# Optimization experiments

Measured on AMD Instinct MI355X. Metric: run time of the kernel, lower is better.

The kernel has to match this reference:

```python
import jax, jax.numpy as jnp
import numpy as np

RADIUS, HEAD, SLOT, DIM = 16.0, 8, 112, 512

def _l2norm(x, axis):
    n = jnp.linalg.norm(x, axis=axis, keepdims=True)
    return x / jnp.maximum(n, 1e-12)

def _layernorm(x, g, b, eps=1e-5):
    mu = jnp.mean(x, axis=-1, keepdims=True)
    var = jnp.mean((x - mu) ** 2, axis=-1, keepdims=True)
    return (x - mu) / jnp.sqrt(var + eps) * g + b

def setup_inputs() -> dict:
    key = jax.random.key(0)
    ks = jax.random.split(key, 12)
    B, S = 32, 512
    return {
        "query": jax.random.normal(ks[0], (B, S, DIM), jnp.float32),
        "value": jax.random.normal(ks[1], (B, S, DIM), jnp.float32),
        "key_mem": jax.random.normal(ks[2], (HEAD * SLOT, DIM // HEAD), jnp.float32) * 0.5,
        "value_mem": jax.random.normal(ks[3], (SLOT, DIM), jnp.float32) * 0.5,
        "Wq": jax.random.normal(ks[4], (DIM, DIM), jnp.float32) * 0.02,
        "bq": jnp.zeros((DIM,), jnp.float32),
        "Wv": jax.random.normal(ks[5], (DIM, DIM), jnp.float32) * 0.02,
        "bv": jnp.zeros((DIM,), jnp.float32),
        "Wl": jax.random.normal(ks[6], (DIM, DIM * HEAD), jnp.float32) * 0.02,
        "bl": jnp.zeros((DIM,), jnp.float32),
        "g1": jnp.ones((DIM,), jnp.float32), "b1": jnp.zeros((DIM,), jnp.float32),
        "g2": jnp.ones((DIM,), jnp.float32), "b2": jnp.zeros((DIM,), jnp.float32),
        "g3": jnp.ones((DIM,), jnp.float32), "b3": jnp.zeros((DIM,), jnp.float32),
    }

def reference(query, value, key_mem, value_mem, Wq, bq, Wv, bv, Wl, bl,
              g1, b1, g2, b2, g3, b3):
    B, S, C = query.shape
    mq = query.reshape(B * S, C)                                   # (BS, 512)
    # --- key addressing (read path) ---
    key_norm = _l2norm(key_mem.reshape(HEAD, SLOT, -1), axis=2)    # (h, s, 64)
    eq = _l2norm((mq @ Wq.T + bq).reshape(B * S, HEAD, -1), axis=2)
    key_sim = jnp.einsum('bhd,hsd->bhs', eq, key_norm)             # (BS, h, s)
    key_add = jax.nn.softmax(RADIUS * key_sim, axis=2)
    m_head = jnp.einsum('bhs,sd->bhd', key_add,
                        jax.lax.stop_gradient(value_mem))          # (BS, h, 512)
    vir = _layernorm(m_head.reshape(B * S, HEAD * DIM) @ Wl.T + bl, g2, b2)
    te_fusion = _layernorm(query + vir.reshape(B, S, DIM), g1, b1)  # dropout = eval identity
    # --- value addressing (write/train path) ---
    mv = value.reshape(B * S, DIM)
    ev = jax.lax.stop_gradient(mv) @ Wv.T + bv
    value_norm = _l2norm(value_mem, axis=1)                        # (s, 512)
    value_sim = _l2norm(ev, axis=1) @ value_norm.T                 # (BS, s)
    value_add = jax.nn.softmax(RADIUS * value_sim, axis=1)
    aud = value_add @ value_mem                                    # (BS, 512)
    contrastive = 0.5 * jnp.abs(jnp.eye(SLOT, dtype=value_norm.dtype)
                                - value_norm @ value_norm.T).sum()[None]
    mvd = jax.lax.stop_gradient(mv)
    cos = (aud * mvd).sum(1) / jnp.maximum(
        jnp.linalg.norm(aud, axis=1) * jnp.linalg.norm(mvd, axis=1), 1e-8)
    recon = jnp.abs(1.0 - cos).reshape(B, S).sum(1)                # (B,)
    aud = _layernorm(aud, g3, b3)
    tr_fusion = _layernorm(query + aud.reshape(B, S, DIM), g1, b1)
    return (te_fusion, tr_fusion, recon, contrastive)
```

## Files before the change

### kernel.cpp

```cpp
#include <hip/hip_runtime.h>
#include <math.h>

#define DIMC   512
#define HEADS  8
#define SLOTS  112
#define HD     64
#define NROWS  16384
#define RADIUSF 16.0f

typedef short short8 __attribute__((ext_vector_type(8)));
typedef unsigned short ushort8 __attribute__((ext_vector_type(8)));
typedef float f32x4  __attribute__((ext_vector_type(4)));

__device__ __forceinline__ unsigned short f2bf(float f)
{
    unsigned u = __float_as_uint(f);
    unsigned r = (u + 0x7FFFu + ((u >> 16) & 1u)) >> 16;
    return (unsigned short)r;
}
__device__ __forceinline__ float bf2f(unsigned short h)
{
    return __uint_as_float((unsigned)h << 16);
}

__device__ __forceinline__ void gl16(const void* g, void* lds_wave_base)
{
    __builtin_amdgcn_global_load_lds(
        (const __attribute__((address_space(1))) unsigned int*)g,
        (__attribute__((address_space(3))) unsigned int*)lds_wave_base,
        16, 0, 0);
}

#define DPP_ADD(x, ctrl, rmask)                                               \
    (x) += __int_as_float(__builtin_amdgcn_update_dpp(                        \
               0, __float_as_int(x), (ctrl), (rmask), 0xf, true))

__device__ __forceinline__ float wsum64(float x)
{
    DPP_ADD(x, 0x111, 0xf);
    DPP_ADD(x, 0x112, 0xf);
    DPP_ADD(x, 0x114, 0xf);
    DPP_ADD(x, 0x118, 0xf);
    DPP_ADD(x, 0x142, 0xa);
    DPP_ADD(x, 0x143, 0xc);
    return __int_as_float(__builtin_amdgcn_readlane(__float_as_int(x), 63));
}

__device__ __forceinline__ void wsum64_4(float& a, float& b, float& c, float& d)
{
    DPP_ADD(a, 0x111, 0xf); DPP_ADD(b, 0x111, 0xf); DPP_ADD(c, 0x111, 0xf); DPP_ADD(d, 0x111, 0xf);
    DPP_ADD(a, 0x112, 0xf); DPP_ADD(b, 0x112, 0xf); DPP_ADD(c, 0x112, 0xf); DPP_ADD(d, 0x112, 0xf);
    DPP_ADD(a, 0x114, 0xf); DPP_ADD(b, 0x114, 0xf); DPP_ADD(c, 0x114, 0xf); DPP_ADD(d, 0x114, 0xf);
    DPP_ADD(a, 0x118, 0xf); DPP_ADD(b, 0x118, 0xf); DPP_ADD(c, 0x118, 0xf); DPP_ADD(d, 0x118, 0xf);
    DPP_ADD(a, 0x142, 0xa); DPP_ADD(b, 0x142, 0xa); DPP_ADD(c, 0x142, 0xa); DPP_ADD(d, 0x142, 0xa);
    DPP_ADD(a, 0x143, 0xc); DPP_ADD(b, 0x143, 0xc); DPP_ADD(c, 0x143, 0xc); DPP_ADD(d, 0x143, 0xc);
    a = __int_as_float(__builtin_amdgcn_readlane(__float_as_int(a), 63));
    b = __int_as_float(__builtin_amdgcn_readlane(__float_as_int(b), 63));
    c = __int_as_float(__builtin_amdgcn_readlane(__float_as_int(c), 63));
    d = __int_as_float(__builtin_amdgcn_readlane(__float_as_int(d), 63));
}

__global__ __launch_bounds__(256)
void gemm_bf16(const short* __restrict__ A, int lda,
               const short* __restrict__ B, int ldb,
               float* __restrict__ C, unsigned short* __restrict__ Cb,
               int ldc, int K, const float* __restrict__ bias, int Nvalid,
               int aZ, int bZ, int cZ)
{
    __shared__ short As[128 * 32];
    __shared__ short Bs[128 * 32];
    A += (size_t)blockIdx.z * aZ;
    B += (size_t)blockIdx.z * bZ;
    const size_t czoff = (size_t)blockIdx.z * cZ;
    const int tid  = threadIdx.x;
    const int wave = tid >> 6;
    const int lane = tid & 63;
    const int m0 = blockIdx.y * 128;
    const int n0 = blockIdx.x * 128;
    const int wm = (wave >> 1) * 64;
    const int wn = (wave & 1) * 64;

    const int srow = tid >> 2;
    const int schk = (tid & 3) * 8;

    const int fr = lane & 15;
    const int fq = (lane >> 4) * 8;

    f32x4 acc[4][4] = {};

    const short* Ag = A + (size_t)(m0 + srow) * lda + schk;
    const short* Bg = B + (size_t)(n0 + srow) * ldb + schk;

    short* asL = As + wave * 512;
    short* asU = As + 2048 + wave * 512;
    short* bsL = Bs + wave * 512;
    short* bsU = Bs + 2048 + wave * 512;

    for (int k0 = 0; k0 < K; k0 += 32) {
        gl16(Ag, asL);
        gl16(Ag + (size_t)64 * lda, asU);
        gl16(Bg, bsL);
        gl16(Bg + (size_t)64 * ldb, bsU);
        Ag += 32; Bg += 32;
        __syncthreads();
        short8 af[4], bf[4];
        #pragma unroll
        for (int i = 0; i < 4; ++i)
            af[i] = *(const short8*)&As[(wm + i * 16 + fr) * 32 + fq];
        #pragma unroll
        for (int j = 0; j < 4; ++j)
            bf[j] = *(const short8*)&Bs[(wn + j * 16 + fr) * 32 + fq];
        #pragma unroll
        for (int i = 0; i < 4; ++i)
            #pragma unroll
            for (int j = 0; j < 4; ++j)
                acc[i][j] = __builtin_amdgcn_mfma_f32_16x16x32_bf16(
                    af[i], bf[j], acc[i][j], 0, 0, 0);
        __syncthreads();
    }

    const int cr = (lane >> 4) * 4;
    const int cc = lane & 15;
    #pragma unroll
    for (int i = 0; i < 4; ++i) {
        const int grow = m0 + wm + i * 16 + cr;
        #pragma unroll
        for (int j = 0; j < 4; ++j) {
            const int gcol = n0 + wn + j * 16 + cc;
            if (gcol < Nvalid) {
                const float bb = bias ? bias[gcol] : 0.f;
                const size_t base = czoff + (size_t)grow * ldc + gcol;
                #pragma unroll
                for (int r = 0; r < 4; ++r) {
                    const float val = acc[i][j][r] + bb;
                    if (C)  C[base + (size_t)r * ldc]  = val;
                    if (Cb) Cb[base + (size_t)r * ldc] = f2bf(val);
                }
            }
        }
    }
}

__global__ __launch_bounds__(256)
void gemm_softmax(const short* __restrict__ A, int lda, int aZ,
                  const short* __restrict__ B, int ldb, int bZ,
                  int K,
                  unsigned short* __restrict__ Ob, int ldo, int oPerZ, int padN)
{
    __shared__ short As[128 * 32];
    __shared__ short Bs[128 * 32];
    __shared__ float P[128][113];
    __shared__ float hinvS[128];
    A += (size_t)blockIdx.z * aZ;
    B += (size_t)blockIdx.z * bZ;
    const int tid  = threadIdx.x;
    const int wave = tid >> 6;
    const int lane = tid & 63;
    const int m0 = blockIdx.y * 128;
    const int wm = (wave >> 1) * 64;
    const int wn = (wave & 1) * 64;
    const int srow = tid >> 2;
    const int schk = (tid & 3) * 8;
    const int fr = lane & 15;
    const int fq = (lane >> 4) * 8;

    f32x4 acc[4][4] = {};
    float ss[4] = {0.f, 0.f, 0.f, 0.f};

    const short* Ag = A + (size_t)(m0 + srow) * lda + schk;
    const short* Bg = B + (size_t)srow * ldb + schk;

    short* asL = As + wave * 512;
    short* asU = As + 2048 + wave * 512;
    short* bsL = Bs + wave * 512;
    short* bsU = Bs + 2048 + wave * 512;

    for (int k0 = 0; k0 < K; k0 += 32) {
        gl16(Ag, asL);
        gl16(Ag + (size_t)64 * lda, asU);
        gl16(Bg, bsL);
        gl16(Bg + (size_t)64 * ldb, bsU);
        Ag += 32; Bg += 32;
        __syncthreads();
        short8 af[4], bf[4];
        #pragma unroll
        for (int i = 0; i < 4; ++i)
            af[i] = *(const short8*)&As[(wm + i * 16 + fr) * 32 + fq];
        #pragma unroll
        for (int j = 0; j < 4; ++j)
            bf[j] = *(const short8*)&Bs[(wn + j * 16 + fr) * 32 + fq];
        #pragma unroll
        for (int i = 0; i < 4; ++i)
            #pragma unroll
            for (int e = 0; e < 8; ++e) {
                const float f = bf2f((unsigned short)af[i][e]);
                ss[i] += f * f;
            }
        #pragma unroll
        for (int i = 0; i < 4; ++i)
            #pragma unroll
            for (int j = 0; j < 4; ++j)
                acc[i][j] = __builtin_amdgcn_mfma_f32_16x16x32_bf16(
                    af[i], bf[j], acc[i][j], 0, 0, 0);
        __syncthreads();
    }

    #pragma unroll
    for (int i = 0; i < 4; ++i) {
        ss[i] += __shfl_xor(ss[i], 16, 64);
        ss[i] += __shfl_xor(ss[i], 32, 64);
    }
    if (lane < 16) {
        #pragma unroll
        for (int i = 0; i < 4; ++i)
            hinvS[wm + i * 16 + lane] = 1.f / fmaxf(sqrtf(ss[i]), 1e-12f);
    }

    const int cr = (lane >> 4) * 4;
    const int cc = lane & 15;
    #pragma unroll
    for (int i = 0; i < 4; ++i) {
        const int prow = wm + i * 16 + cr;
        #pragma unroll
        for (int j = 0; j < 4; ++j) {
            const int pcol = wn + j * 16 + cc;
            if (pcol < SLOTS) {
                #pragma unroll
                for (int r = 0; r < 4; ++r)
                    P[prow + r][pcol] = acc[i][j][r];
            }
        }
    }
    __syncthreads();

    const int rowt = tid >> 1;
    const int half = tid & 1;
    const int k0 = half * 56;
    const int rr = m0 + rowt;
    const float s = RADIUSF * hinvS[rowt];
    float mx = -1e30f;
    for (int k = k0; k < k0 + 56; ++k) mx = fmaxf(mx, P[rowt][k]);
    mx = fmaxf(mx, __shfl_xor(mx, 1, 64));
    float sum = 0.f;
    for (int k = k0; k < k0 + 56; ++k) {
        const float e = __expf(s * (P[rowt][k] - mx));
        P[rowt][k] = e;
        sum += e;
    }
    sum += __shfl_xor(sum, 1, 64);
    const float inv = 1.f / sum;
    unsigned short* orow = Ob + (size_t)rr * ldo + (size_t)blockIdx.z * oPerZ;
    for (int k = k0; k < k0 + 56; ++k) orow[k] = f2bf(P[rowt][k] * inv);
    if (half == 1)
        for (int k = SLOTS; k < padN; ++k) orow[k] = 0;
}


#define FUSED_GEMM_CORE(A, lda, B, ldb, K)                                    \
    f32x4 acc[2][8] = {};                                                     \
    {                                                                         \
        const int lrow = lane >> 2;                                           \
        const int lchk = (lane & 3) * 8;                                      \
        const short* Ag = (A) + (size_t)(m0 + wave * 16 + lrow) * (lda) + lchk;\
        const short* Bg = (B) + (size_t)(wave * 16 + lrow) * (ldb) + lchk;    \
        short* asB = As + wave * 512;                                         \
        short* bsB = Bs + wave * 512;                                         \
        for (int k0 = 0; k0 < (K); k0 += 32) {                                \
            if (wave < 2) gl16(Ag, asB);                                      \
            _Pragma("unroll")                                                 \
            for (int s = 0; s < 8; ++s)                                       \
                gl16(Bg + (size_t)(s * 64) * (ldb), bsB + s * 2048);          \
            Ag += 32; Bg += 32;                                               \
            __syncthreads();                                                  \
            short8 af[2], bf[8];                                              \
            af[0] = *(const short8*)&As[fr * 32 + fq];                        \
            af[1] = *(const short8*)&As[(16 + fr) * 32 + fq];                 \
            _Pragma("unroll")                                                 \
            for (int c = 0; c < 8; ++c)                                       \
                bf[c] = *(const short8*)&Bs[(wave * 128 + c * 16 + fr) * 32 + fq];\
            _Pragma("unroll")                                                 \
            for (int i = 0; i < 2; ++i)                                       \
                _Pragma("unroll")                                             \
                for (int c = 0; c < 8; ++c)                                   \
                    acc[i][c] = __builtin_amdgcn_mfma_f32_16x16x32_bf16(      \
                        af[i], bf[c], acc[i][c], 0, 0, 0);                    \
            __syncthreads();                                                  \
        }                                                                     \
    }                                                                         \
    {                                                                         \
        const int cr = (lane >> 4) * 4;                                       \
        const int cc = lane & 15;                                             \
        _Pragma("unroll")                                                     \
        for (int i = 0; i < 2; ++i)                                           \
            _Pragma("unroll")                                                 \
            for (int c = 0; c < 8; ++c) {                                     \
                const int col = wave * 128 + c * 16 + cc;                     \
                _Pragma("unroll")                                             \
                for (int r = 0; r < 4; ++r)                                   \
                    P[(i * 16 + cr + r) * 516 + col] = acc[i][c][r];          \
            }                                                                 \
    }                                                                         \
    __syncthreads();

__global__ __launch_bounds__(256)
void gemm_vir_te(const short* __restrict__ A, int lda,
                 const short* __restrict__ B, int ldb, int K,
                 const float* __restrict__ bias, const float* __restrict__ query,
                 const float* __restrict__ g1, const float* __restrict__ b1,
                 const float* __restrict__ g2, const float* __restrict__ b2,
                 float* __restrict__ out_te)
{
    __shared__ float P[32 * 516];
    short* As = (short*)P;
    short* Bs = As + 1024;
    const int tid = threadIdx.x;
    const int wave = tid >> 6;
    const int lane = tid & 63;
    const int m0 = blockIdx.x * 32;
    const int fr = lane & 15;
    const int fq = (lane >> 4) * 8;

    FUSED_GEMM_CORE(A, lda, B, ldb, K)

    const int c0 = lane * 8;
    float blv[8], gg2[8], bb2[8], gg1[8], bb1[8];
    *(f32x4*)&blv[0] = *(const f32x4*)(bias + c0);
    *(f32x4*)&blv[4] = *(const f32x4*)(bias + c0 + 4);
    *(f32x4*)&gg2[0] = *(const f32x4*)(g2 + c0);
    *(f32x4*)&gg2[4] = *(const f32x4*)(g2 + c0 + 4);
    *(f32x4*)&bb2[0] = *(const f32x4*)(b2 + c0);
    *(f32x4*)&bb2[4] = *(const f32x4*)(b2 + c0 + 4);
    *(f32x4*)&gg1[0] = *(const f32x4*)(g1 + c0);
    *(f32x4*)&gg1[4] = *(const f32x4*)(g1 + c0 + 4);
    *(f32x4*)&bb1[0] = *(const f32x4*)(b1 + c0);
    *(f32x4*)&bb1[4] = *(const f32x4*)(b1 + c0 + 4);

    for (int rp = 0; rp < 4; ++rp) {
        const int lr0 = rp * 8 + wave * 2;
        float x[2][8], q[2][8];
        #pragma unroll
        for (int p = 0; p < 2; ++p) {
            *(f32x4*)&x[p][0] = *(const f32x4*)&P[(lr0 + p) * 516 + c0];
            *(f32x4*)&x[p][4] = *(const f32x4*)&P[(lr0 + p) * 516 + c0 + 4];
            const size_t gbase = (size_t)(m0 + lr0 + p) * DIMC + c0;
            *(f32x4*)&q[p][0] = *(const f32x4*)(query + gbase);
            *(f32x4*)&q[p][4] = *(const f32x4*)(query + gbase + 4);
            #pragma unroll
            for (int j = 0; j < 8; ++j) x[p][j] += blv[j];
        }
        float s1[2] = {0.f, 0.f}, s2[2] = {0.f, 0.f};
        #pragma unroll
        for (int p = 0; p < 2; ++p)
            #pragma unroll
            for (int j = 0; j < 8; ++j) {
                s1[p] += x[p][j];
                s2[p] += x[p][j] * x[p][j];
            }
        wsum64_4(s1[0], s2[0], s1[1], s2[1]);

        float y[2][8];
        float t1[2] = {0.f, 0.f}, t2[2] = {0.f, 0.f};
        #pragma unroll
        for (int p = 0; p < 2; ++p) {
            const float mu = s1[p] * (1.f / DIMC);
            const float var = s2[p] * (1.f / DIMC) - mu * mu;
            const float rstd = rsqrtf(var + 1e-5f);
            #pragma unroll
            for (int j = 0; j < 8; ++j) {
                const float v = (x[p][j] - mu) * rstd * gg2[j] + bb2[j];
                y[p][j] = q[p][j] + v;
                t1[p] += y[p][j];
                t2[p] += y[p][j] * y[p][j];
            }
        }
        wsum64_4(t1[0], t2[0], t1[1], t2[1]);

        #pragma unroll
        for (int p = 0; p < 2; ++p) {
            const float mu = t1[p] * (1.f / DIMC);
            const float var = t2[p] * (1.f / DIMC) - mu * mu;
            const float rstd = rsqrtf(var + 1e-5f);
            float o[8];
            #pragma unroll
            for (int j = 0; j < 8; ++j)
                o[j] = (y[p][j] - mu) * rstd * gg1[j] + bb1[j];
            const size_t gbase = (size_t)(m0 + lr0 + p) * DIMC + c0;
            *(float4*)(out_te + gbase)     = make_float4(o[0], o[1], o[2], o[3]);
            *(float4*)(out_te + gbase + 4) = make_float4(o[4], o[5], o[6], o[7]);
        }
    }
}

__global__ __launch_bounds__(256)
void gemm_aud_tr(const short* __restrict__ A, int lda,
                 const short* __restrict__ B, int ldb, int K,
                 const float* __restrict__ value, const float* __restrict__ query,
                 const float* __restrict__ g1, const float* __restrict__ b1,
                 const float* __restrict__ g3, const float* __restrict__ b3,
                 float* __restrict__ out_tr, float* __restrict__ recon)
{
    __shared__ float P[32 * 516];
    __shared__ float red[4];
    short* As = (short*)P;
    short* Bs = As + 1024;
    const int tid = threadIdx.x;
    const int wave = tid >> 6;
    const int lane = tid & 63;
    const int m0 = blockIdx.x * 32;
    const int fr = lane & 15;
    const int fq = (lane >> 4) * 8;

    FUSED_GEMM_CORE(A, lda, B, ldb, K)

    const int c0 = lane * 8;
    float gg3[8], bb3[8], gg1[8], bb1[8];
    *(f32x4*)&gg3[0] = *(const f32x4*)(g3 + c0);
    *(f32x4*)&gg3[4] = *(const f32x4*)(g3 + c0 + 4);
    *(f32x4*)&bb3[0] = *(const f32x4*)(b3 + c0);
    *(f32x4*)&bb3[4] = *(const f32x4*)(b3 + c0 + 4);
    *(f32x4*)&gg1[0] = *(const f32x4*)(g1 + c0);
    *(f32x4*)&gg1[4] = *(const f32x4*)(g1 + c0 + 4);
    *(f32x4*)&bb1[0] = *(const f32x4*)(b1 + c0);
    *(f32x4*)&bb1[4] = *(const f32x4*)(b1 + c0 + 4);

    float rloc = 0.f;
    for (int rp = 0; rp < 4; ++rp) {
        const int lr0 = rp * 8 + wave * 2;
        float a[2][8], v[2][8], q[2][8];
        #pragma unroll
        for (int p = 0; p < 2; ++p) {
            *(f32x4*)&a[p][0] = *(const f32x4*)&P[(lr0 + p) * 516 + c0];
            *(f32x4*)&a[p][4] = *(const f32x4*)&P[(lr0 + p) * 516 + c0 + 4];
            const size_t gbase = (size_t)(m0 + lr0 + p) * DIMC + c0;
            *(f32x4*)&v[p][0] = *(const f32x4*)(value + gbase);
            *(f32x4*)&v[p][4] = *(const f32x4*)(value + gbase + 4);
            *(f32x4*)&q[p][0] = *(const f32x4*)(query + gbase);
            *(f32x4*)&q[p][4] = *(const f32x4*)(query + gbase + 4);
        }
        float dot[2] = {0.f, 0.f}, na[2] = {0.f, 0.f};
        float nv[2] = {0.f, 0.f}, s1[2] = {0.f, 0.f};
        #pragma unroll
        for (int p = 0; p < 2; ++p)
            #pragma unroll
            for (int j = 0; j < 8; ++j) {
                dot[p] += a[p][j] * v[p][j];
                na[p]  += a[p][j] * a[p][j];
                nv[p]  += v[p][j] * v[p][j];
                s1[p]  += a[p][j];
            }
        wsum64_4(dot[0], na[0], nv[0], s1[0]);
        wsum64_4(dot[1], na[1], nv[1], s1[1]);

        #pragma unroll
        for (int p = 0; p < 2; ++p) {
            const float cosv = dot[p] / fmaxf(sqrtf(na[p]) * sqrtf(nv[p]), 1e-8f);
            rloc += fabsf(1.f - cosv);
        }

        float y[2][8];
        float t1[2] = {0.f, 0.f}, t2[2] = {0.f, 0.f};
        #pragma unroll
        for (int p = 0; p < 2; ++p) {
            const float mu = s1[p] * (1.f / DIMC);
            const float var = na[p] * (1.f / DIMC) - mu * mu;
            const float rstd = rsqrtf(var + 1e-5f);
            #pragma unroll
            for (int j = 0; j < 8; ++j) {
                const float w = (a[p][j] - mu) * rstd * gg3[j] + bb3[j];
                y[p][j] = q[p][j] + w;
                t1[p] += y[p][j];
                t2[p] += y[p][j] * y[p][j];
            }
        }
        wsum64_4(t1[0], t2[0], t1[1], t2[1]);

        #pragma unroll
        for (int p = 0; p < 2; ++p) {
            const float mu = t1[p] * (1.f / DIMC);
            const float var = t2[p] * (1.f / DIMC) - mu * mu;
            const float rstd = rsqrtf(var + 1e-5f);
            float o[8];
            #pragma unroll
            for (int j = 0; j < 8; ++j)
                o[j] = (y[p][j] - mu) * rstd * gg1[j] + bb1[j];
            const size_t gbase = (size_t)(m0 + lr0 + p) * DIMC + c0;
            *(float4*)(out_tr + gbase)     = make_float4(o[0], o[1], o[2], o[3]);
            *(float4*)(out_tr + gbase + 4) = make_float4(o[4], o[5], o[6], o[7]);
        }
    }

    if (lane == 0) red[wave] = rloc;
    __syncthreads();
    if (tid == 0)
        atomicAdd(&recon[m0 >> 9], red[0] + red[1] + red[2] + red[3]);
}

__device__ __forceinline__ float block_sum_256(float v, float* red)
{
    #pragma unroll
    for (int off = 32; off; off >>= 1) v += __shfl_down(v, off, 64);
    const int lane = threadIdx.x & 63, wid = threadIdx.x >> 6;
    __syncthreads();
    if (lane == 0) red[wid] = v;
    __syncthreads();
    return red[0] + red[1] + red[2] + red[3];
}

__global__ void conv_all(const float* __restrict__ q, const float* __restrict__ v,
                         const float* __restrict__ Wq, const float* __restrict__ Wv,
                         const float* __restrict__ Wl, const float* __restrict__ vm,
                         unsigned short* __restrict__ qbf, unsigned short* __restrict__ vbf,
                         unsigned short* __restrict__ wqbf, unsigned short* __restrict__ wvbf,
                         unsigned short* __restrict__ wlbf, unsigned short* __restrict__ vmbf)
{
    const int i = blockIdx.x * blockDim.x + threadIdx.x;
    const float* src;
    unsigned short* dst;
    int off;
    if (i < 2097152)      { src = q;  dst = qbf;  off = i; }
    else if (i < 4194304) { src = v;  dst = vbf;  off = i - 2097152; }
    else if (i < 4259840) { src = Wq; dst = wqbf; off = i - 4194304; }
    else if (i < 4325376) { src = Wv; dst = wvbf; off = i - 4259840; }
    else if (i < 4849664) { src = Wl; dst = wlbf; off = i - 4325376; }
    else if (i < 4864000) { src = vm; dst = vmbf; off = i - 4849664; }
    else {
        const int j = i - 4864000;
        *(ushort4*)(vmbf + 57344 + (size_t)j * 4) = make_ushort4(0, 0, 0, 0);
        return;
    }
    const float4 x = *(const float4*)(src + (size_t)off * 4);
    ushort4 o;
    o.x = f2bf(x.x); o.y = f2bf(x.y); o.z = f2bf(x.z); o.w = f2bf(x.w);
    *(ushort4*)(dst + (size_t)off * 4) = o;
}

__global__ void prep_key_norm(const float* __restrict__ km,
                              unsigned short* __restrict__ knb,
                              float* __restrict__ outrc)
{
    const int row = blockIdx.x;
    const int h = row >> 7, s = row & 127;
    const int lane = threadIdx.x;
    if (row == 0 && lane < 33) outrc[lane] = 0.f;
    const float v = (s < SLOTS) ? km[(size_t)(h * SLOTS + s) * HD + lane] : 0.f;
    const float ssum = wsum64(v * v);
    const float inv = 1.f / fmaxf(sqrtf(ssum), 1e-12f);
    knb[(size_t)row * HD + lane] = f2bf(v * inv);
}

__global__ void prep_value_norm(const float* __restrict__ vm,
                                float* __restrict__ vn,
                                unsigned short* __restrict__ vnb,
                                unsigned short* __restrict__ vmTb)
{
    const int row = blockIdx.x;
    const int tid = threadIdx.x;
    if (row >= 112) {
        const int idx = (row - 112) * 256 + tid;
        if (idx < 8192) {
            vmTb[(size_t)(idx >> 4) * 128 + 112 + (idx & 15)] = 0;
        } else {
            const int j = idx - 8192;
            vnb[(size_t)(112 + (j >> 9)) * 512 + (j & 511)] = 0;
        }
        return;
    }
    __shared__ float red[4];
    const float v0 = vm[(size_t)row * DIMC + tid];
    const float v1 = vm[(size_t)row * DIMC + 256 + tid];
    const float tot = block_sum_256(v0 * v0 + v1 * v1, red);
    const float inv = 1.f / fmaxf(sqrtf(tot), 1e-12f);
    vn[(size_t)row * DIMC + tid]        = v0 * inv;
    vn[(size_t)row * DIMC + 256 + tid]  = v1 * inv;
    vnb[(size_t)row * DIMC + tid]       = f2bf(v0 * inv);
    vnb[(size_t)row * DIMC + 256 + tid] = f2bf(v1 * inv);
    vmTb[(size_t)tid * 128 + row]         = f2bf(v0);
    vmTb[(size_t)(256 + tid) * 128 + row] = f2bf(v1);
}

__global__ void contrastive_kernel(const float* __restrict__ vn, float* __restrict__ outc)
{
    __shared__ float vni[DIMC];
    __shared__ float red[2];
    const int i = blockIdx.x, tid = threadIdx.x;
    for (int d = tid; d < DIMC; d += 128) vni[d] = vn[(size_t)i * DIMC + d];
    __syncthreads();
    float t = 0.f;
    if (tid < SLOTS) {
        const float* r = vn + (size_t)tid * DIMC;
        float dot = 0.f;
        for (int d = 0; d < DIMC; ++d) dot += vni[d] * r[d];
        const float delta = (tid == i) ? 1.f : 0.f;
        t = fabsf(delta - dot);
    }
    #pragma unroll
    for (int off = 32; off; off >>= 1) t += __shfl_down(t, off, 64);
    if ((tid & 63) == 0) red[tid >> 6] = t;
    __syncthreads();
    if (tid == 0) atomicAdd(outc, 0.5f * (red[0] + red[1]));
}

extern "C" void kernel_launch(void* const* d_in, const int* in_sizes, int n_in,
                              void* d_out, int out_size, void* d_ws, size_t ws_size,
                              hipStream_t stream)
{
    const float* query = (const float*)d_in[0];
    const float* value = (const float*)d_in[1];
    const float* keym  = (const float*)d_in[2];
    const float* vmem  = (const float*)d_in[3];
    const float* Wq    = (const float*)d_in[4];
    const float* bq    = (const float*)d_in[5];
    const float* Wv    = (const float*)d_in[6];
    const float* bv    = (const float*)d_in[7];
    const float* Wl    = (const float*)d_in[8];
    const float* bl    = (const float*)d_in[9];
    const float* g1    = (const float*)d_in[10];
    const float* b1    = (const float*)d_in[11];
    const float* g2    = (const float*)d_in[12];
    const float* b2    = (const float*)d_in[13];
    const float* g3    = (const float*)d_in[14];
    const float* b3    = (const float*)d_in[15];

    float* out    = (float*)d_out;
    float* out_te = out;
    float* out_tr = out + 8388608;
    float* out_rc = out + 16777216;

    float* ws = (float*)d_ws;
    unsigned short* w_knb  = (unsigned short*)(ws + 0);
    unsigned short* w_vmTb = (unsigned short*)(ws + 32768);
    unsigned short* w_vnb  = (unsigned short*)(ws + 65536);
    float*          w_vn   = ws + 98304;
    unsigned short* w_w2tbf= (unsigned short*)(ws + 155648);
    unsigned short* w_vmbf = (unsigned short*)(ws + 385024);
    unsigned short* w_wlbf = (unsigned short*)(ws + 417792);
    unsigned short* w_xbf  = (unsigned short*)(ws + 1466368);
    unsigned short* w_kaddc= (unsigned short*)(ws + 5660672);
    unsigned short* w_vsb  = (unsigned short*)(ws + 13000704);
    unsigned short* w_qbf  = (unsigned short*)(ws + 14049280);
    unsigned short* w_vbf  = (unsigned short*)(ws + 18243584);
    unsigned short* w_wqbf = (unsigned short*)(ws + 22437888);
    unsigned short* w_wvbf = (unsigned short*)(ws + 22568960);

    conv_all<<<19008, 256, 0, stream>>>(query, value, Wq, Wv, Wl, vmem,
                                        w_qbf, w_vbf, w_wqbf, w_wvbf,
                                        w_wlbf, w_vmbf);
    prep_key_norm<<<1024, 64, 0, stream>>>(keym, w_knb, out_rc);
    prep_value_norm<<<176, 256, 0, stream>>>(vmem, w_vn, w_vnb, w_vmTb);
    contrastive_kernel<<<112, 128, 0, stream>>>(w_vn, out_rc + 32);
    gemm_bf16<<<dim3(1, 4, 8), 256, 0, stream>>>(
        (const short*)w_wlbf, HEADS * DIMC, (const short*)w_vmbf, DIMC,
        nullptr, w_w2tbf, HEADS * SLOTS, DIMC, nullptr, SLOTS,
        DIMC, 0, SLOTS);

    gemm_bf16<<<dim3(4, 128), 256, 0, stream>>>(
        (const short*)w_qbf, DIMC, (const short*)w_wqbf, DIMC,
        nullptr, w_xbf, DIMC, DIMC, bq, DIMC, 0, 0, 0);
    gemm_softmax<<<dim3(1, 128, 8), 256, 0, stream>>>(
        (const short*)w_xbf, DIMC, HD, (const short*)w_knb, HD, 128 * HD,
        HD, w_kaddc, HEADS * SLOTS, SLOTS, SLOTS);
    gemm_vir_te<<<NROWS / 32, 256, 0, stream>>>(
        (const short*)w_kaddc, HEADS * SLOTS, (const short*)w_w2tbf, HEADS * SLOTS,
        HEADS * SLOTS, bl, query, g1, b1, g2, b2, out_te);

    gemm_bf16<<<dim3(4, 128), 256, 0, stream>>>(
        (const short*)w_vbf, DIMC, (const short*)w_wvbf, DIMC,
        nullptr, w_xbf, DIMC, DIMC, bv, DIMC, 0, 0, 0);
    gemm_softmax<<<dim3(1, 128, 1), 256, 0, stream>>>(
        (const short*)w_xbf, DIMC, 0, (const short*)w_vnb, DIMC, 0,
        DIMC, w_vsb, 128, 0, 128);
    gemm_aud_tr<<<NROWS / 32, 256, 0, stream>>>(
        (const short*)w_vsb, 128, (const short*)w_vmTb, 128, 128,
        value, query, g1, b1, g3, b3, out_tr, out_rc);
}
```

Measured before the change: 336.8 us.

## Use 512-thread blocks with K=64 steps in fused GEMM+layernorm kernels

The fused GEMM-plus-layernorm kernels (vir/te and aud/tr) now run with 512 threads (8 waves) per block instead of 256. Each wave computes 64 output columns instead of 128, and each iteration loads a K-step of 64 into two LDS buffers, halving the number of barriers per K. The goal is less per-wave register pressure, more waves for latency hiding, and fewer sync points. In exchange, LDS use per block grows to about 68KB, which limits how many blocks fit on a CU, and the epilogue row mapping and recon reduction are adjusted to eight waves.

```diff
diff --git a/kernel.cpp b/kernel.cpp
--- a/kernel.cpp
+++ b/kernel.cpp
@@ -255,35 +255,55 @@
         for (int k = SLOTS; k < padN; ++k) orow[k] = 0;
 }
 
-
-#define FUSED_GEMM_CORE(A, lda, B, ldb, K)                                    \
-    f32x4 acc[2][8] = {};                                                     \
+#define FUSED_LDS_DECL                                                        \
+    __shared__ float U[17408];    \
+    float* P = U;                                                             \
+    short* As0 = (short*)U;                             \
+    short* As1 = As0 + 1024;                            \
+    short* Bs0 = As1 + 1024;                           \
+    short* Bs1 = Bs0 + 16384;
+
+#define FUSED_GEMM_CORE(Aptr, lda, Bptr, ldb, K)                              \
+    f32x4 acc[2][4] = {};                                                     \
     {                                                                         \
         const int lrow = lane >> 2;                                           \
         const int lchk = (lane & 3) * 8;                                      \
-        const short* Ag = (A) + (size_t)(m0 + wave * 16 + lrow) * (lda) + lchk;\
-        const short* Bg = (B) + (size_t)(wave * 16 + lrow) * (ldb) + lchk;    \
-        short* asB = As + wave * 512;                                         \
-        short* bsB = Bs + wave * 512;                                         \
-        for (int k0 = 0; k0 < (K); k0 += 32) {                                \
-            if (wave < 2) gl16(Ag, asB);                                      \
+        for (int k0 = 0; k0 < (K); k0 += 64) {                                \
+            if (wave < 2)                                                     \
+                gl16((Aptr) + (size_t)(m0 + wave * 16 + lrow) * (lda) + k0 + lchk, \
+                     As0 + wave * 512);                                       \
+            else if (wave < 4)                                                \
+                gl16((Aptr) + (size_t)(m0 + (wave - 2) * 16 + lrow) * (lda) + k0 + 32 + lchk, \
+                     As1 + (wave - 2) * 512);                                 \
             _Pragma("unroll")                                                 \
-            for (int s = 0; s < 8; ++s)                                       \
-                gl16(Bg + (size_t)(s * 64) * (ldb), bsB + s * 2048);          \
-            Ag += 32; Bg += 32;                                               \
+            for (int s = 0; s < 4; ++s) {                                     \
+                const size_t brow = (size_t)(wave * 64 + s * 16 + lrow);      \
+                gl16((Bptr) + brow * (ldb) + k0 + lchk,                       \
+                     Bs0 + (wave * 64 + s * 16) * 32);                        \
+                gl16((Bptr) + brow * (ldb) + k0 + 32 + lchk,                  \
+                     Bs1 + (wave * 64 + s * 16) * 32);                        \
+            }                                                                 \
             __syncthreads();                                                  \
-            short8 af[2], bf[8];                                              \
-            af[0] = *(const short8*)&As[fr * 32 + fq];                        \
-            af[1] = *(const short8*)&As[(16 + fr) * 32 + fq];                 \
+            short8 af0[2], af1[2], bf0[4], bf1[4];                            \
             _Pragma("unroll")                                                 \
-            for (int c = 0; c < 8; ++c)                                       \
-                bf[c] = *(const short8*)&Bs[(wave * 128 + c * 16 + fr) * 32 + fq];\
+            for (int i = 0; i < 2; ++i) {                                     \
+                af0[i] = *(const short8*)&As0[(i * 16 + fr) * 32 + fq];       \
+                af1[i] = *(const short8*)&As1[(i * 16 + fr) * 32 + fq];       \
+            }                                                                 \
+            _Pragma("unroll")                                                 \
+            for (int c = 0; c < 4; ++c) {                                     \
+                bf0[c] = *(const short8*)&Bs0[(wave * 64 + c * 16 + fr) * 32 + fq]; \
+                bf1[c] = *(const short8*)&Bs1[(wave * 64 + c * 16 + fr) * 32 + fq]; \
+            }                                                                 \
             _Pragma("unroll")                                                 \
             for (int i = 0; i < 2; ++i)                                       \
                 _Pragma("unroll")                                             \
-                for (int c = 0; c < 8; ++c)                                   \
+                for (int c = 0; c < 4; ++c) {                                 \
                     acc[i][c] = __builtin_amdgcn_mfma_f32_16x16x32_bf16(      \
-                        af[i], bf[c], acc[i][c], 0, 0, 0);                    \
+                        af0[i], bf0[c], acc[i][c], 0, 0, 0);                  \
+                    acc[i][c] = __builtin_amdgcn_mfma_f32_16x16x32_bf16(      \
+                        af1[i], bf1[c], acc[i][c], 0, 0, 0);                  \
+                }                                                             \
             __syncthreads();                                                  \
         }                                                                     \
     }                                                                         \
@@ -293,8 +313,8 @@
         _Pragma("unroll")                                                     \
         for (int i = 0; i < 2; ++i)                                           \
             _Pragma("unroll")                                                 \
-            for (int c = 0; c < 8; ++c) {                                     \
-                const int col = wave * 128 + c * 16 + cc;                     \
+            for (int c = 0; c < 4; ++c) {                                     \
+                const int col = wave * 64 + c * 16 + cc;                      \
                 _Pragma("unroll")                                             \
                 for (int r = 0; r < 4; ++r)                                   \
                     P[(i * 16 + cr + r) * 516 + col] = acc[i][c][r];          \
@@ -302,7 +322,7 @@
     }                                                                         \
     __syncthreads();
 
-__global__ __launch_bounds__(256)
+__global__ __launch_bounds__(512, 4)
 void gemm_vir_te(const short* __restrict__ A, int lda,
                  const short* __restrict__ B, int ldb, int K,
                  const float* __restrict__ bias, const float* __restrict__ query,
@@ -310,9 +330,7 @@
                  const float* __restrict__ g2, const float* __restrict__ b2,
                  float* __restrict__ out_te)
 {
-    __shared__ float P[32 * 516];
-    short* As = (short*)P;
-    short* Bs = As + 1024;
+    FUSED_LDS_DECL
     const int tid = threadIdx.x;
     const int wave = tid >> 6;
     const int lane = tid & 63;
@@ -335,8 +353,8 @@
     *(f32x4*)&bb1[0] = *(const f32x4*)(b1 + c0);
     *(f32x4*)&bb1[4] = *(const f32x4*)(b1 + c0 + 4);
 
-    for (int rp = 0; rp < 4; ++rp) {
-        const int lr0 = rp * 8 + wave * 2;
+    for (int rp = 0; rp < 2; ++rp) {
+        const int lr0 = wave * 4 + rp * 2;
         float x[2][8], q[2][8];
         #pragma unroll
         for (int p = 0; p < 2; ++p) {
@@ -391,7 +409,7 @@
     }
 }
 
-__global__ __launch_bounds__(256)
+__global__ __launch_bounds__(512, 4)
 void gemm_aud_tr(const short* __restrict__ A, int lda,
                  const short* __restrict__ B, int ldb, int K,
                  const float* __restrict__ value, const float* __restrict__ query,
@@ -399,10 +417,8 @@
                  const float* __restrict__ g3, const float* __restrict__ b3,
                  float* __restrict__ out_tr, float* __restrict__ recon)
 {
-    __shared__ float P[32 * 516];
-    __shared__ float red[4];
-    short* As = (short*)P;
-    short* Bs = As + 1024;
+    FUSED_LDS_DECL
+    __shared__ float red[8];
     const int tid = threadIdx.x;
     const int wave = tid >> 6;
     const int lane = tid & 63;
@@ -424,8 +440,8 @@
     *(f32x4*)&bb1[4] = *(const f32x4*)(b1 + c0 + 4);
 
     float rloc = 0.f;
-    for (int rp = 0; rp < 4; ++rp) {
-        const int lr0 = rp * 8 + wave * 2;
+    for (int rp = 0; rp < 2; ++rp) {
+        const int lr0 = wave * 4 + rp * 2;
         float a[2][8], v[2][8], q[2][8];
         #pragma unroll
         for (int p = 0; p < 2; ++p) {
@@ -492,7 +508,8 @@
     if (lane == 0) red[wave] = rloc;
     __syncthreads();
     if (tid == 0)
-        atomicAdd(&recon[m0 >> 9], red[0] + red[1] + red[2] + red[3]);
+        atomicAdd(&recon[m0 >> 9], red[0] + red[1] + red[2] + red[3]
+                                 + red[4] + red[5] + red[6] + red[7]);
 }
 
 __device__ __forceinline__ float block_sum_256(float v, float* red)
@@ -659,7 +676,7 @@
     gemm_softmax<<<dim3(1, 128, 8), 256, 0, stream>>>(
         (const short*)w_xbf, DIMC, HD, (const short*)w_knb, HD, 128 * HD,
         HD, w_kaddc, HEADS * SLOTS, SLOTS, SLOTS);
-    gemm_vir_te<<<NROWS / 32, 256, 0, stream>>>(
+    gemm_vir_te<<<NROWS / 32, 512, 0, stream>>>(
         (const short*)w_kaddc, HEADS * SLOTS, (const short*)w_w2tbf, HEADS * SLOTS,
         HEADS * SLOTS, bl, query, g1, b1, g2, b2, out_te);
 
@@ -669,7 +686,7 @@
     gemm_softmax<<<dim3(1, 128, 1), 256, 0, stream>>>(
         (const short*)w_xbf, DIMC, 0, (const short*)w_vnb, DIMC, 0,
         DIMC, w_vsb, 128, 0, 128);
-    gemm_aud_tr<<<NROWS / 32, 256, 0, stream>>>(
+    gemm_aud_tr<<<NROWS / 32, 512, 0, stream>>>(
         (const short*)w_vsb, 128, (const short*)w_vmTb, 128, 128,
         value, query, g1, b1, g3, b3, out_tr, out_rc);
 }
```

Measured after the change: 329.4 us, median of 2. 2.2% less time.
